# Optimization experiments

Measured on AMD Instinct MI355X. Metric: run time of the kernel, lower is better.

## Reference

```python
import jax, jax.numpy as jnp
import numpy as np

N = 100000
E = 1600000
IN_C, HID_C, OUT_C = 128, 128, 64


def setup_inputs() -> dict:
    key = jax.random.key(0)
    ks = jax.random.split(key, 8)
    x = jax.random.normal(ks[0], (N, IN_C), dtype=jnp.float32)
    edge_index = jax.random.randint(ks[1], (2, E), 0, N, dtype=jnp.int64)
    s_in = 1.0 / np.sqrt(IN_C)
    s_hid = 1.0 / np.sqrt(HID_C)
    w1l = jax.random.uniform(ks[2], (HID_C, IN_C), jnp.float32, -s_in, s_in)
    w1r = jax.random.uniform(ks[3], (HID_C, IN_C), jnp.float32, -s_in, s_in)
    b1 = jnp.zeros((HID_C,), jnp.float32)
    w2l = jax.random.uniform(ks[4], (OUT_C, HID_C), jnp.float32, -s_hid, s_hid)
    w2r = jax.random.uniform(ks[5], (OUT_C, HID_C), jnp.float32, -s_hid, s_hid)
    b2 = jnp.zeros((OUT_C,), jnp.float32)
    return {"x": x, "edge_index": edge_index, "w1l": w1l, "w1r": w1r,
            "b1": b1, "w2l": w2l, "w2r": w2r, "b2": b2}


def _sage_conv(x, src, dst, wl, wr, b):
    # mean aggregation of neighbor messages x[src] at dst
    agg = jax.ops.segment_sum(x[src], dst, num_segments=N)  # [N, d]
    deg = jax.ops.segment_sum(jnp.ones((src.shape[0],), x.dtype), dst, num_segments=N)
    agg = agg / jnp.maximum(deg, 1.0)[:, None]
    # PyG SAGEConv: lin_l(agg) + lin_r(x); lin_l carries the bias
    return agg @ wl.T + b + x @ wr.T


def reference(x, edge_index, w1l, w1r, b1, w2l, w2r, b2):
    src, dst = edge_index[0], edge_index[1]
    h = jax.nn.relu(_sage_conv(x, src, dst, w1l, w1r, b1))
    z = _sage_conv(h, src, dst, w2l, w2r, b2)  # [N, OUT_C]
    # decode: gather node pairs, elementwise multiply + reduce -> [E]
    return jnp.sum(z[src] * z[dst], axis=1)
```

## Files before the change

### kernel.cpp

```cpp
#include <hip/hip_runtime.h>


#define IN_C      128
#define HID_C     128
#define OUT_C     64
#define NPART     8
#define SLICE_E   4096
#define CAP       64

typedef unsigned short u16;
typedef __attribute__((ext_vector_type(8))) __bf16 bf16x8;
typedef __attribute__((ext_vector_type(4))) float f32x4;
typedef __attribute__((ext_vector_type(4))) int i32x4;

__device__ inline u16 f2bf(float f) {
    unsigned u = __float_as_uint(f);
    u += 0x7fff + ((u >> 16) & 1);
    return (u16)(u >> 16);
}
__device__ inline float bflo(unsigned v) { return __uint_as_float(v << 16); }
__device__ inline float bfhi(unsigned v) { return __uint_as_float(v & 0xffff0000u); }

__global__ __launch_bounds__(256) void fill_pad(const int* __restrict__ ei,
                                                int* __restrict__ cnt,
                                                int* __restrict__ csr, int E, int n) {
    const int range = blockIdx.x & (NPART - 1);
    const int slice = blockIdx.x >> 3;
    const int nr = (n + NPART - 1) / NPART;
    const int lo = range * nr;
    const int hi = min(n, lo + nr);
    const int base = slice * SLICE_E;
    const int e1 = min(E, base + SLICE_E);
    for (int e = base + threadIdx.x * 4; e < e1; e += 1024) {
        i32x4 d4 = __builtin_nontemporal_load((const i32x4*)(ei + (size_t)E + e));
#pragma unroll
        for (int j = 0; j < 4; ++j) {
            int d = d4[j];
            if (d >= lo && d < hi) {
                int s = __builtin_nontemporal_load(ei + e + j);
                int r = atomicAdd(&cnt[d], 1);
                if (r < CAP && (unsigned)s < (unsigned)n)
                    csr[(size_t)d * CAP + r] = s;
            }
        }
    }
}

__global__ __launch_bounds__(256) void deg_inv(const int* __restrict__ cnt,
                                               float* __restrict__ inv_deg, int n) {
    int i = blockIdx.x * 256 + threadIdx.x;
    if (i < n) inv_deg[i] = 1.0f / (float)max(cnt[i], 1);
}

__global__ __launch_bounds__(256) void cvt_x(const float* __restrict__ in,
                                             u16* __restrict__ outb, int n4) {
    int i = blockIdx.x * 256 + threadIdx.x;
    if (i >= n4) return;
    float4 v = ((const float4*)in)[i];
    ushort4 o;
    o.x = f2bf(v.x); o.y = f2bf(v.y); o.z = f2bf(v.z); o.w = f2bf(v.w);
    ((ushort4*)outb)[i] = o;
}

__global__ __launch_bounds__(256) void cvt_w(const float* __restrict__ w1l,
                                             const float* __restrict__ w1r,
                                             const float* __restrict__ w2l,
                                             const float* __restrict__ w2r,
                                             u16* __restrict__ Wb1,
                                             u16* __restrict__ Wb2) {
    int i = blockIdx.x * 256 + threadIdx.x;
    if (i < 32768) {
        int c = i >> 8, k = i & 255;
        float v = (k < 128) ? w1l[c * 128 + k] : w1r[c * 128 + (k - 128)];
        Wb1[i] = f2bf(v);
    } else if (i < 49152) {
        int j = i - 32768;
        float v = (j < 8192) ? w2l[j] : w2r[j - 8192];
        Wb2[j] = f2bf(v);
    }
}

__global__ __launch_bounds__(256) void gemm_l1(const u16* __restrict__ A0,
                                               const u16* __restrict__ A1,
                                               const u16* __restrict__ Wb,
                                               const float* __restrict__ bias,
                                               u16* __restrict__ outp, int nrows) {
    constexpr int K    = 256;
    constexpr int COLS = 128;
    constexpr int KS   = K / 32;
    constexpr int NCT  = COLS / 16;
    constexpr int WROW = K + 8;
    __shared__ u16 wl[COLS * WROW];

    const int t = threadIdx.x;
    for (int i = t; i < COLS * (K / 8); i += 256) {
        int r = i >> 5, p = i & 31;
        *(uint4*)&wl[r * WROW + p * 8] = *(const uint4*)&Wb[(size_t)r * K + p * 8];
    }
    __syncthreads();

    const int wv    = t >> 6;
    const int lane  = t & 63;
    const int cl    = lane & 15;
    const int quad  = lane >> 4;
    const int rbase = blockIdx.x * 128 + wv * 32;

    bf16x8 afrag[2][KS];
#pragma unroll
    for (int tile = 0; tile < 2; ++tile) {
        int r = min(rbase + tile * 16 + cl, nrows - 1);
        const u16* s0 = A0 + (size_t)r * 128 + quad * 8;
        const u16* s1 = A1 + (size_t)r * 128 + quad * 8;
#pragma unroll
        for (int ks = 0; ks < 4; ++ks) {
            afrag[tile][ks]     = *(const bf16x8*)(s0 + ks * 32);
            afrag[tile][4 + ks] = *(const bf16x8*)(s1 + ks * 32);
        }
    }

#pragma unroll
    for (int ct = 0; ct < NCT; ++ct) {
        f32x4 acc0 = {0.f, 0.f, 0.f, 0.f};
        f32x4 acc1 = {0.f, 0.f, 0.f, 0.f};
        const u16* wp = &wl[(ct * 16 + cl) * WROW + quad * 8];
#pragma unroll
        for (int ks = 0; ks < KS; ++ks) {
            bf16x8 bfrag = *(const bf16x8*)(wp + ks * 32);
            acc0 = __builtin_amdgcn_mfma_f32_16x16x32_bf16(afrag[0][ks], bfrag, acc0, 0, 0, 0);
            acc1 = __builtin_amdgcn_mfma_f32_16x16x32_bf16(afrag[1][ks], bfrag, acc1, 0, 0, 0);
        }
        int gc = ct * 16 + cl;
        float bv = bias[gc];
#pragma unroll
        for (int tile = 0; tile < 2; ++tile) {
            f32x4 a = tile ? acc1 : acc0;
#pragma unroll
            for (int r = 0; r < 4; ++r) {
                int row = rbase + tile * 16 + quad * 4 + r;
                if (row < nrows)
                    outp[(size_t)row * COLS + gc] = f2bf(fmaxf(a[r] + bv, 0.f));
            }
        }
    }
}

template <int K, int COLS>
__global__ __launch_bounds__(256) void gemm_mfma(const u16* __restrict__ xb,
                                                 const u16* __restrict__ Wb,
                                                 const float* __restrict__ bias,
                                                 u16* __restrict__ outA,
                                                 u16* __restrict__ outB,
                                                 int nrows) {
    constexpr int NCOL = 2 * COLS;
    constexpr int NCT  = NCOL / 16;
    constexpr int KS   = K / 32;
    constexpr int WROW = K + 8;
    __shared__ u16 wl[NCOL * WROW];

    const int t = threadIdx.x;
    for (int i = t; i < NCOL * (K / 8); i += 256) {
        int r = i / (K / 8), p = i % (K / 8);
        *(uint4*)&wl[r * WROW + p * 8] = *(const uint4*)&Wb[(size_t)r * K + p * 8];
    }
    __syncthreads();

    const int wv    = t >> 6;
    const int lane  = t & 63;
    const int cl    = lane & 15;
    const int quad  = lane >> 4;
    const int rbase = blockIdx.x * 128 + wv * 32;

    bf16x8 afrag[2][KS];
#pragma unroll
    for (int tile = 0; tile < 2; ++tile) {
        int r = rbase + tile * 16 + cl;
        const u16* src = xb + (size_t)min(r, nrows - 1) * K + quad * 8;
#pragma unroll
        for (int ks = 0; ks < KS; ++ks)
            afrag[tile][ks] = *(const bf16x8*)(src + ks * 32);
    }

#pragma unroll
    for (int ct = 0; ct < NCT; ++ct) {
        f32x4 acc0 = {0.f, 0.f, 0.f, 0.f};
        f32x4 acc1 = {0.f, 0.f, 0.f, 0.f};
        const u16* wp = &wl[(ct * 16 + cl) * WROW + quad * 8];
#pragma unroll
        for (int ks = 0; ks < KS; ++ks) {
            bf16x8 bfrag = *(const bf16x8*)(wp + ks * 32);
            acc0 = __builtin_amdgcn_mfma_f32_16x16x32_bf16(afrag[0][ks], bfrag, acc0, 0, 0, 0);
            acc1 = __builtin_amdgcn_mfma_f32_16x16x32_bf16(afrag[1][ks], bfrag, acc1, 0, 0, 0);
        }
        int gc = ct * 16 + cl;
        bool isA = gc < COLS;
        float bv = isA ? 0.f : bias[gc - COLS];
        u16* dst = isA ? (outA + gc) : (outB + (gc - COLS));
#pragma unroll
        for (int tile = 0; tile < 2; ++tile) {
            f32x4 a = tile ? acc1 : acc0;
#pragma unroll
            for (int r = 0; r < 4; ++r) {
                int row = rbase + tile * 16 + quad * 4 + r;
                if (row < nrows) dst[(size_t)row * COLS] = f2bf(a[r] + bv);
            }
        }
    }
}

template <int C, bool HAS_OTHER>
__global__ __launch_bounds__(256) void agg_bf(const u16* __restrict__ gl,
                                              const u16* __restrict__ other,
                                              const int* __restrict__ cnt,
                                              const int* __restrict__ csr,
                                              const float* __restrict__ inv_deg,
                                              u16* __restrict__ outp, int n) {
    constexpr int G = C / 8;
    int t = threadIdx.x;
    int node = blockIdx.x * (256 / G) + t / G;
    int l = t % G;
    if (node >= n) return;

    int deg = min(cnt[node], CAP);
    const int* sp = csr + (size_t)node * CAP;
    float a[8] = {0.f, 0.f, 0.f, 0.f, 0.f, 0.f, 0.f, 0.f};
    const size_t coff = (size_t)l * 8;
    for (int p = 0; p < deg; ++p) {
        int s = sp[p];
        uint4 v = *(const uint4*)(gl + (size_t)s * C + coff);
        a[0] += bflo(v.x); a[1] += bfhi(v.x);
        a[2] += bflo(v.y); a[3] += bfhi(v.y);
        a[4] += bflo(v.z); a[5] += bfhi(v.z);
        a[6] += bflo(v.w); a[7] += bfhi(v.w);
    }
    float id = inv_deg[node];
    float r[8];
    if (HAS_OTHER) {
        uint4 o = *(const uint4*)(other + (size_t)node * C + coff);
        r[0] = fmaf(a[0], id, bflo(o.x)); r[1] = fmaf(a[1], id, bfhi(o.x));
        r[2] = fmaf(a[2], id, bflo(o.y)); r[3] = fmaf(a[3], id, bfhi(o.y));
        r[4] = fmaf(a[4], id, bflo(o.z)); r[5] = fmaf(a[5], id, bfhi(o.z));
        r[6] = fmaf(a[6], id, bflo(o.w)); r[7] = fmaf(a[7], id, bfhi(o.w));
    } else {
#pragma unroll
        for (int j = 0; j < 8; ++j) r[j] = a[j] * id;
    }
    uint4 w;
    w.x = (unsigned)f2bf(r[0]) | ((unsigned)f2bf(r[1]) << 16);
    w.y = (unsigned)f2bf(r[2]) | ((unsigned)f2bf(r[3]) << 16);
    w.z = (unsigned)f2bf(r[4]) | ((unsigned)f2bf(r[5]) << 16);
    w.w = (unsigned)f2bf(r[6]) | ((unsigned)f2bf(r[7]) << 16);
    *(uint4*)(outp + (size_t)node * C + coff) = w;
}

__global__ __launch_bounds__(256) void decode(const u16* __restrict__ z,
                                              const int* __restrict__ ei,
                                              float* __restrict__ out, int E, int n) {
    int t = blockIdx.x * 256 + threadIdx.x;
    int e = t >> 3, l = t & 7;
    if (e >= E) return;
    int s = __builtin_nontemporal_load(ei + e);
    int d = __builtin_nontemporal_load(ei + (size_t)E + e);
    float p = 0.f;
    if ((unsigned)s < (unsigned)n && (unsigned)d < (unsigned)n) {
        uint4 a = *(const uint4*)(z + (size_t)s * OUT_C + l * 8);
        uint4 b = *(const uint4*)(z + (size_t)d * OUT_C + l * 8);
        p  = bflo(a.x) * bflo(b.x) + bfhi(a.x) * bfhi(b.x);
        p += bflo(a.y) * bflo(b.y) + bfhi(a.y) * bfhi(b.y);
        p += bflo(a.z) * bflo(b.z) + bfhi(a.z) * bfhi(b.z);
        p += bflo(a.w) * bflo(b.w) + bfhi(a.w) * bfhi(b.w);
    }
    p += __shfl_xor(p, 4);
    p += __shfl_xor(p, 2);
    p += __shfl_xor(p, 1);
    if (l == 0) out[e] = p;
}

extern "C" void kernel_launch(void* const* d_in, const int* in_sizes, int n_in,
                              void* d_out, int out_size, void* d_ws, size_t ws_size,
                              hipStream_t stream) {
    const float* x   = (const float*)d_in[0];
    const int*   ei  = (const int*)d_in[1];
    const float* w1l = (const float*)d_in[2];
    const float* w1r = (const float*)d_in[3];
    const float* b1  = (const float*)d_in[4];
    const float* w2l = (const float*)d_in[5];
    const float* w2r = (const float*)d_in[6];
    const float* b2  = (const float*)d_in[7];
    float*       out = (float*)d_out;

    const int N = in_sizes[0] / IN_C;
    const int E = in_sizes[1] / 2;

    auto alignup = [](size_t v) { return (v + 255) & ~(size_t)255; };
    char* p = (char*)d_ws;
    int*   cnt       = (int*)p;   p += alignup((size_t)N * 4);
    float* inv_deg   = (float*)p; p += alignup((size_t)N * 4);
    int*   csr       = (int*)p;   p += alignup((size_t)N * CAP * 4);
    u16*   Wb1       = (u16*)p;   p += alignup((size_t)HID_C * 2 * IN_C * 2);
    u16*   Wb2       = (u16*)p;   p += alignup((size_t)2 * OUT_C * HID_C * 2);
    u16*   xb        = (u16*)p;   p += alignup((size_t)N * IN_C * 2);
    u16*   ag1       = (u16*)p;   p += alignup((size_t)N * HID_C * 2);
    u16*   hb        = (u16*)p;   p += alignup((size_t)N * HID_C * 2);
    u16*   hlb       = xb;
    u16*   hrb       = xb + (size_t)N * OUT_C;
    u16*   zb        = ag1;

    const int nslice = (E + SLICE_E - 1) / SLICE_E;

    cvt_x<<<(N * IN_C / 4 + 255) / 256, 256, 0, stream>>>(x, xb, N * IN_C / 4);
    cvt_w<<<192, 256, 0, stream>>>(w1l, w1r, w2l, w2r, Wb1, Wb2);

    hipMemsetAsync(cnt, 0, (size_t)N * 4, stream);
    fill_pad<<<nslice * NPART, 256, 0, stream>>>(ei, cnt, csr, E, N);
    deg_inv<<<(N + 255) / 256, 256, 0, stream>>>(cnt, inv_deg, N);

    const int rb = (N + 127) / 128;

    agg_bf<HID_C, false><<<(N + 15) / 16, 256, 0, stream>>>(xb, nullptr, cnt, csr,
                                                            inv_deg, ag1, N);
    gemm_l1<<<rb, 256, 0, stream>>>(ag1, xb, Wb1, b1, hb, N);

    gemm_mfma<HID_C, OUT_C><<<rb, 256, 0, stream>>>(hb, Wb2, b2, hlb, hrb, N);
    agg_bf<OUT_C, true><<<(N + 31) / 32, 256, 0, stream>>>(hlb, hrb, cnt, csr,
                                                           inv_deg, zb, N);

    decode<<<((size_t)E * 8 + 255) / 256, 256, 0, stream>>>(zb, ei, out, E, N);
}
```

Measured before the change: 414.8 us.

## Bucket edges by destination range before filling padded CSR

Replaces the single CSR fill kernel with two passes. Previously each of eight destination-range partitions re-read the whole edge list. Now one pass reads each edge once and uses wave-ballot aggregated atomics to scatter (src,dst) pairs into per-range, per-replica buckets. A second kernel walks the buckets and does the per-node count atomics and CSR writes. This removes the eightfold re-read of the edge list, at the cost of writing and reading an intermediate bucket buffer. Any bucket that exceeds its fixed capacity silently drops edges.

```diff
diff --git a/kernel.cpp b/kernel.cpp
--- a/kernel.cpp
+++ b/kernel.cpp
@@ -5,13 +5,16 @@
 #define HID_C     128
 #define OUT_C     64
 #define NPART     8
-#define SLICE_E   4096
+#define NREP      32
+#define SUBCAP    8192
+#define BPB       4
 #define CAP       64
 
 typedef unsigned short u16;
 typedef __attribute__((ext_vector_type(8))) __bf16 bf16x8;
 typedef __attribute__((ext_vector_type(4))) float f32x4;
 typedef __attribute__((ext_vector_type(4))) int i32x4;
+typedef __attribute__((ext_vector_type(2))) int i32x2;
 
 __device__ inline u16 f2bf(float f) {
     unsigned u = __float_as_uint(f);
@@ -21,28 +24,78 @@
 __device__ inline float bflo(unsigned v) { return __uint_as_float(v << 16); }
 __device__ inline float bfhi(unsigned v) { return __uint_as_float(v & 0xffff0000u); }
 
-__global__ __launch_bounds__(256) void fill_pad(const int* __restrict__ ei,
-                                                int* __restrict__ cnt,
-                                                int* __restrict__ csr, int E, int n) {
-    const int range = blockIdx.x & (NPART - 1);
-    const int slice = blockIdx.x >> 3;
-    const int nr = (n + NPART - 1) / NPART;
-    const int lo = range * nr;
-    const int hi = min(n, lo + nr);
-    const int base = slice * SLICE_E;
-    const int e1 = min(E, base + SLICE_E);
-    for (int e = base + threadIdx.x * 4; e < e1; e += 1024) {
-        i32x4 d4 = __builtin_nontemporal_load((const i32x4*)(ei + (size_t)E + e));
-#pragma unroll
-        for (int j = 0; j < 4; ++j) {
-            int d = d4[j];
-            if (d >= lo && d < hi) {
-                int s = __builtin_nontemporal_load(ei + e + j);
-                int r = atomicAdd(&cnt[d], 1);
-                if (r < CAP && (unsigned)s < (unsigned)n)
-                    csr[(size_t)d * CAP + r] = s;
+__global__ __launch_bounds__(256) void bucket_edges(const int* __restrict__ ei,
+                                                    int* __restrict__ bcur,
+                                                    i32x2* __restrict__ bkt,
+                                                    int E, int n) {
+    const int rep  = blockIdx.x & (NREP - 1);
+    const int nr   = (n + NPART - 1) / NPART;
+    const int lane = threadIdx.x & 63;
+    const int base = blockIdx.x * 1024 + threadIdx.x * 4;
+
+    i32x4 d4 = {-1, -1, -1, -1}, s4 = {0, 0, 0, 0};
+    if (base < E) {
+        d4 = __builtin_nontemporal_load((const i32x4*)(ei + (size_t)E + base));
+        s4 = __builtin_nontemporal_load((const i32x4*)(ei + base));
+    }
+
+#pragma unroll
+    for (int j = 0; j < 4; ++j) {
+        int d = d4[j], s = s4[j];
+        int b = ((unsigned)d < (unsigned)n && (unsigned)s < (unsigned)n)
+                    ? (int)((unsigned)d / (unsigned)nr) : -1;
+#pragma unroll
+        for (int bb = 0; bb < NPART; ++bb) {
+            bool m = (b == bb);
+            unsigned long long mask = __ballot(m);
+            if (mask == 0ull) continue;
+            int cntm   = __popcll(mask);
+            int leader = __ffsll((long long)mask) - 1;
+            int bofs = 0;
+            if (lane == leader) bofs = atomicAdd(&bcur[bb * NREP + rep], cntm);
+            bofs = __shfl(bofs, leader);
+            if (m) {
+                int off = bofs + __popcll(mask & ((1ull << lane) - 1ull));
+                if (off < SUBCAP) {
+                    i32x2 v; v.x = s; v.y = d;
+                    bkt[(size_t)(bb * NREP + rep) * SUBCAP + off] = v;
+                }
             }
         }
+    }
+}
+
+__global__ __launch_bounds__(256) void fill_from_bkt(const i32x2* __restrict__ bkt,
+                                                     const int* __restrict__ bcur,
+                                                     int* __restrict__ cnt,
+                                                     int* __restrict__ csr, int n) {
+    const int b     = blockIdx.x & (NPART - 1);
+    const int t     = blockIdx.x >> 3;
+    const int r     = t & (NREP - 1);
+    const int chunk = t >> 5;
+    const int idx   = b * NREP + r;
+    const int m     = min(bcur[idx], SUBCAP);
+    const int per   = (m + BPB - 1) / BPB;
+    const int lo    = chunk * per;
+    const int hi    = min(m, lo + per);
+    const i32x2* sp = bkt + (size_t)idx * SUBCAP;
+
+    for (int i0 = lo + threadIdx.x * 4; i0 < hi; i0 += 1024) {
+        int kmax = min(4, hi - i0);
+        i32x2 ev[4];
+#pragma unroll
+        for (int k = 0; k < 4; ++k)
+            if (k < kmax) ev[k] = __builtin_nontemporal_load(&sp[i0 + k]);
+        int rk[4];
+#pragma unroll
+        for (int k = 0; k < 4; ++k)
+            if (k < kmax) rk[k] = atomicAdd(&cnt[ev[k].y], 1);
+#pragma unroll
+        for (int k = 0; k < 4; ++k)
+            if (k < kmax) {
+                int rr = rk[k];
+                if (rr < CAP) csr[(size_t)ev[k].y * CAP + rr] = ev[k].x;
+            }
     }
 }
 
@@ -295,7 +348,9 @@
     char* p = (char*)d_ws;
     int*   cnt       = (int*)p;   p += alignup((size_t)N * 4);
     float* inv_deg   = (float*)p; p += alignup((size_t)N * 4);
+    int*   bcur      = (int*)p;   p += alignup((size_t)NPART * NREP * 4);
     int*   csr       = (int*)p;   p += alignup((size_t)N * CAP * 4);
+    i32x2* bkt       = (i32x2*)p; p += alignup((size_t)NPART * NREP * SUBCAP * 8);
     u16*   Wb1       = (u16*)p;   p += alignup((size_t)HID_C * 2 * IN_C * 2);
     u16*   Wb2       = (u16*)p;   p += alignup((size_t)2 * OUT_C * HID_C * 2);
     u16*   xb        = (u16*)p;   p += alignup((size_t)N * IN_C * 2);
@@ -305,13 +360,14 @@
     u16*   hrb       = xb + (size_t)N * OUT_C;
     u16*   zb        = ag1;
 
-    const int nslice = (E + SLICE_E - 1) / SLICE_E;
-
     cvt_x<<<(N * IN_C / 4 + 255) / 256, 256, 0, stream>>>(x, xb, N * IN_C / 4);
     cvt_w<<<192, 256, 0, stream>>>(w1l, w1r, w2l, w2r, Wb1, Wb2);
 
     hipMemsetAsync(cnt, 0, (size_t)N * 4, stream);
-    fill_pad<<<nslice * NPART, 256, 0, stream>>>(ei, cnt, csr, E, N);
+    hipMemsetAsync(bcur, 0, (size_t)NPART * NREP * 4, stream);
+    const int nblk1 = (E + 1023) / 1024;
+    bucket_edges<<<nblk1, 256, 0, stream>>>(ei, bcur, bkt, E, N);
+    fill_from_bkt<<<NPART * NREP * BPB, 256, 0, stream>>>(bkt, bcur, cnt, csr, N);
     deg_inv<<<(N + 255) / 256, 256, 0, stream>>>(cnt, inv_deg, N);
 
     const int rb = (N + 127) / 128;
```

New measurement: 742.1 us. +78.9%, slower.
